# Performance work log

Measured on AMD Instinct MI355X. Metric: run time of the kernel, lower is better.

The kernel has to match this reference:

```python
import jax, jax.numpy as jnp
import numpy as np

IN_FEATURES = 896
OUT_FEATURES = 151936  # Qwen2.5 vocab
BATCH, SEQ = 2, 1024


def setup_inputs() -> dict:
    key = jax.random.key(0)
    k1, k2, k3 = jax.random.split(key, 3)
    x = jax.random.normal(k1, (BATCH, SEQ, IN_FEATURES), dtype=jnp.float32)
    # int8-range quantized weights stored as int32 (values in [-127, 127])
    quant_weight = jax.random.randint(k2, (OUT_FEATURES, IN_FEATURES), -127, 128, dtype=jnp.int32)
    # per-output-row scales (positive, small)
    scales = jax.random.uniform(k3, (OUT_FEATURES,), dtype=jnp.float32, minval=0.001, maxval=0.02)
    return {"x": x, "quant_weight": quant_weight, "scales": scales}


def reference(x, quant_weight, scales):
    # dequantize: W = int8_weight * per_row_scale  -> [out, in]
    w = quant_weight.astype(x.dtype) * scales.astype(x.dtype)[:, None]
    # F.linear(x, W, None) == x @ W.T : [b, s, in] x [out, in] -> [b, s, out]
    return jnp.einsum('bsi,oi->bso', x, w)
```

## Files before the change

kernel.cpp:

```cpp
#include <hip/hip_runtime.h>
#include <hip/hip_bf16.h>


#define M_DIM 2048
#define N_DIM 151936
#define K_DIM 896

#define BM 128
#define BN 128
#define BK 64
#define NKT (K_DIM / BK)
#define MB_CNT (M_DIM / BM)
#define NB_CNT (N_DIM / BN)
#define NWG (MB_CNT * NB_CNT)

typedef __attribute__((ext_vector_type(8))) short bf16x8;
typedef __attribute__((ext_vector_type(4))) float f32x4;
typedef __attribute__((ext_vector_type(4))) int   i32x4;
typedef __attribute__((ext_vector_type(4))) unsigned int u32x4;
typedef __attribute__((ext_vector_type(2))) unsigned int u32x2;

static __device__ __forceinline__ unsigned short f2bf(float f) {
    unsigned int u = __builtin_bit_cast(unsigned int, f);
    u += 0x7FFFu + ((u >> 16) & 1u);
    return (unsigned short)(u >> 16);
}
static __device__ __forceinline__ unsigned int pack2(float lo, float hi) {
    return (unsigned int)f2bf(lo) | ((unsigned int)f2bf(hi) << 16);
}
static __device__ __forceinline__ void gload_lds16(const void* g, void* l) {
    __builtin_amdgcn_global_load_lds(
        (const __attribute__((address_space(1))) unsigned int*)g,
        (__attribute__((address_space(3))) unsigned int*)l, 16, 0, 0);
}


__global__ void quant_x_kernel(const float* __restrict__ X,
                               signed char* __restrict__ Xq,
                               float* __restrict__ Sx) {
    const int row  = blockIdx.x * 4 + (threadIdx.x >> 6);
    const int lane = threadIdx.x & 63;
    const float* xr = X + (size_t)row * K_DIM;
    float v[14];
    float am = 0.f;
    #pragma unroll
    for (int i = 0; i < 14; ++i) {
        v[i] = xr[lane + i * 64];
        am = fmaxf(am, fabsf(v[i]));
    }
    #pragma unroll
    for (int off = 32; off > 0; off >>= 1)
        am = fmaxf(am, __shfl_xor(am, off));
    am = fmaxf(am, 1e-20f);
    const float inv = 127.f / am;
    if (lane == 0) Sx[row] = am / 127.f;
    signed char* qr = Xq + (size_t)row * K_DIM;
    #pragma unroll
    for (int i = 0; i < 14; ++i)
        qr[lane + i * 64] = (signed char)(int)rintf(v[i] * inv);
}

__global__ void cvt_w8_kernel(const int* __restrict__ Wq,
                              signed char* __restrict__ W8) {
    const long n8 = (long)N_DIM * K_DIM / 8;
    for (long i = (long)blockIdx.x * blockDim.x + threadIdx.x; i < n8;
         i += (long)gridDim.x * blockDim.x) {
        i32x4 a = ((const i32x4*)Wq)[2 * i];
        i32x4 b = ((const i32x4*)Wq)[2 * i + 1];
        unsigned int lo = (unsigned int)(a[0] & 0xff) |
                          ((unsigned int)(a[1] & 0xff) << 8) |
                          ((unsigned int)(a[2] & 0xff) << 16) |
                          ((unsigned int)(a[3] & 0xff) << 24);
        unsigned int hi = (unsigned int)(b[0] & 0xff) |
                          ((unsigned int)(b[1] & 0xff) << 8) |
                          ((unsigned int)(b[2] & 0xff) << 16) |
                          ((unsigned int)(b[3] & 0xff) << 24);
        u32x2 o; o[0] = lo; o[1] = hi;
        ((u32x2*)W8)[i] = o;
    }
}


#define SCHED0 __builtin_amdgcn_sched_barrier(0)
#define VMCNT(N) asm volatile("s_waitcnt vmcnt(" #N ")" ::: "memory")
#define LGKM0    asm volatile("s_waitcnt lgkmcnt(0)" ::: "memory")

__global__ __launch_bounds__(256, 3)
void lmhead_gemm_i8(const signed char* __restrict__ Xq,
                    const signed char* __restrict__ W8,
                    const float* __restrict__ Sw,
                    const float* __restrict__ Sx,
                    float* __restrict__ O)
{
    __shared__ signed char lds[3][2][BM][BK];

    const int tid  = threadIdx.x;
    const int lane = tid & 63;
    const int wave = tid >> 6;
    const int wr   = wave >> 1;
    const int wc   = wave & 1;

    const int bid = blockIdx.x;
    const int wg  = (bid & 7) * (NWG / 8) + (bid >> 3);
    const int mb  = wg % MB_CNT;
    const int nb  = wg / MB_CNT;

    const int lslot = (lane & 3) ^ ((lane >> 3) & 3);
    const signed char* srcA0 =
        Xq + (size_t)(mb * BM + wave * 16 + (lane >> 2)) * K_DIM + lslot * 16;
    const signed char* srcA1 = srcA0 + (size_t)64 * K_DIM;
    const signed char* srcB0 =
        W8 + (size_t)(nb * BN + wave * 16 + (lane >> 2)) * K_DIM + lslot * 16;
    const signed char* srcB1 = srcB0 + (size_t)64 * K_DIM;

    auto stage = [&](int b3, int k0) {
        gload_lds16(srcA0 + k0, &lds[b3][0][wave * 16][0]);
        gload_lds16(srcA1 + k0, &lds[b3][0][64 + wave * 16][0]);
        gload_lds16(srcB0 + k0, &lds[b3][1][wave * 16][0]);
        gload_lds16(srcB1 + k0, &lds[b3][1][64 + wave * 16][0]);
    };

    const int physoff   = ((lane >> 4) ^ ((lane >> 1) & 3)) * 16;
    const int arow_base = wr * 64 + (lane & 15);
    const int brow_base = wc * 64 + (lane & 15);

    i32x4 acc[4][4];
    #pragma unroll
    for (int i = 0; i < 4; ++i)
        #pragma unroll
        for (int j = 0; j < 4; ++j)
            acc[i][j] = i32x4{0, 0, 0, 0};

    stage(0, 0);
    stage(1, BK);
    SCHED0;
    VMCNT(0);
    SCHED0;
    __builtin_amdgcn_s_barrier();
    SCHED0;

    i32x4 af[2], bfr[4];

#define READ_A(B3, Q) do { \
    _Pragma("unroll") \
    for (int mf = 0; mf < 2; ++mf) \
        af[mf] = *(const i32x4*)&lds[B3][0][arow_base + (Q)*32 + mf*16][physoff]; \
} while (0)
#define READ_B(B3) do { \
    _Pragma("unroll") \
    for (int nf = 0; nf < 4; ++nf) \
        bfr[nf] = *(const i32x4*)&lds[B3][1][brow_base + nf*16][physoff]; \
} while (0)
#define MFMA_Q(Q) do { \
    __builtin_amdgcn_s_setprio(1); \
    _Pragma("unroll") \
    for (int mf = 0; mf < 2; ++mf) { \
        _Pragma("unroll") \
        for (int nf = 0; nf < 4; ++nf) \
            acc[(Q)*2 + mf][nf] = __builtin_amdgcn_mfma_i32_16x16x64_i8( \
                af[mf], bfr[nf], acc[(Q)*2 + mf][nf], 0, 0, 0); \
    } \
    __builtin_amdgcn_s_setprio(0); \
} while (0)
#define BAR_A() do { SCHED0; __builtin_amdgcn_s_barrier(); SCHED0; } while (0)
#define BAR_B() do { SCHED0; LGKM0; SCHED0; __builtin_amdgcn_s_barrier(); SCHED0; } while (0)

    for (int t = 0; t < NKT - 2; ++t) {
        const int cur = t % 3;
        READ_A(cur, 0); READ_B(cur);
        stage((t + 2) % 3, (t + 2) * BK);
        BAR_A();
        MFMA_Q(0);
        BAR_B();
        READ_A(cur, 1);
        SCHED0;
        VMCNT(4);
        BAR_A();
        MFMA_Q(1);
        BAR_B();
    }

    {
        const int cur = (NKT - 2) % 3;
        READ_A(cur, 0); READ_B(cur);
        BAR_A();
        MFMA_Q(0);
        BAR_B();
        READ_A(cur, 1);
        SCHED0;
        VMCNT(0);
        BAR_A();
        MFMA_Q(1);
        BAR_B();
    }
    {
        const int cur = (NKT - 1) % 3;
        READ_A(cur, 0); READ_B(cur);
        BAR_A();
        MFMA_Q(0);
        BAR_B();
        READ_A(cur, 1);
        BAR_A();
        MFMA_Q(1);
    }

#undef READ_A
#undef READ_B
#undef MFMA_Q
#undef BAR_A
#undef BAR_B

    __syncthreads();

    float* lf = (float*)&lds[0][0][0][0];
    const int qw = lane >> 4;
    const int li = lane & 15;

    float scn[4];
    #pragma unroll
    for (int nf = 0; nf < 4; ++nf)
        scn[nf] = Sw[nb * BN + wc * 64 + nf * 16 + li];

    #pragma unroll
    for (int p = 0; p < 2; ++p) {
        if (p) __syncthreads();
        if (wr == p) {
            #pragma unroll
            for (int a = 0; a < 4; ++a) {
                #pragma unroll
                for (int nf = 0; nf < 4; ++nf) {
                    #pragma unroll
                    for (int r = 0; r < 4; ++r) {
                        const int lr   = a * 16 + qw * 4 + r;
                        const int col  = wc * 64 + nf * 16 + li;
                        const int pcol = col ^ (qw << 4);
                        lf[lr * 128 + pcol] = (float)acc[a][nf][r] * scn[nf];
                    }
                }
            }
        }
        __syncthreads();
        #pragma unroll
        for (int i = 0; i < 8; ++i) {
            const int row = wave * 16 + i * 2 + (lane >> 5);
            const int q   = (row >> 2) & 3;
            const int pch = (lane & 31) ^ (q << 2);
            f32x4 v = *(const f32x4*)&lf[row * 128 + pch * 4];
            const size_t grow = (size_t)(mb * BM + p * 64 + row);
            const float sxr = Sx[grow];
            v *= sxr;
            const size_t gcol = (size_t)(nb * BN + (lane & 31) * 4);
            *(f32x4*)&O[grow * N_DIM + gcol] = v;
        }
    }
}


#define FBM 128
#define FBN 128
#define FBK 32
#define FNSTEPS (K_DIM / FBK)
#define FMB (M_DIM / FBM)
#define FNB (N_DIM / FBN)
#define FNWG (FMB * FNB)

__global__ __launch_bounds__(256, 2)
void lmhead_gemm_conv(const float* __restrict__ X,
                      const int* __restrict__ Wq,
                      const float* __restrict__ S,
                      float* __restrict__ O)
{
    __shared__ unsigned short Alds[2][FBM][FBK];
    __shared__ unsigned short Blds2[2][FBN][FBK];

    const int tid  = threadIdx.x;
    const int lane = tid & 63;
    const int wave = tid >> 6;
    const int wr   = wave >> 1;
    const int wc   = wave & 1;

    const int bid = blockIdx.x;
    const int wg  = (bid & 7) * (FNWG / 8) + (bid >> 3);
    const int mb  = wg % FMB;
    const int nb  = wg / FMB;

    const int srow = tid >> 1;
    const int skh  = (tid & 1) * 16;

    const float* aptr = X  + (size_t)(mb * FBM + srow) * K_DIM + skh;
    const int*   wptr = Wq + (size_t)(nb * FBN + srow) * K_DIM + skh;

    f32x4 av[4];
    i32x4 wv[4];

    auto load_tiles = [&](int k0) {
        const f32x4* ap = (const f32x4*)(aptr + k0);
        const i32x4* wp = (const i32x4*)(wptr + k0);
        av[0] = ap[0]; av[1] = ap[1]; av[2] = ap[2]; av[3] = ap[3];
        wv[0] = wp[0]; wv[1] = wp[1]; wv[2] = wp[2]; wv[3] = wp[3];
    };

    auto stage = [&](int buf) {
        unsigned int apk[8], wpk[8];
        #pragma unroll
        for (int i = 0; i < 8; ++i) {
            apk[i] = pack2(av[(2*i) >> 2][(2*i) & 3], av[(2*i+1) >> 2][(2*i+1) & 3]);
            wpk[i] = pack2((float)wv[(2*i) >> 2][(2*i) & 3], (float)wv[(2*i+1) >> 2][(2*i+1) & 3]);
        }
        *(u32x4*)&Alds[buf][srow][skh]      = u32x4{apk[0], apk[1], apk[2], apk[3]};
        *(u32x4*)&Alds[buf][srow][skh + 8]  = u32x4{apk[4], apk[5], apk[6], apk[7]};
        *(u32x4*)&Blds2[buf][srow][skh]     = u32x4{wpk[0], wpk[1], wpk[2], wpk[3]};
        *(u32x4*)&Blds2[buf][srow][skh + 8] = u32x4{wpk[4], wpk[5], wpk[6], wpk[7]};
    };

    f32x4 acc[4][4];
    #pragma unroll
    for (int i = 0; i < 4; ++i)
        #pragma unroll
        for (int j = 0; j < 4; ++j)
            acc[i][j] = f32x4{0.f, 0.f, 0.f, 0.f};

    load_tiles(0);
    stage(0);
    __syncthreads();

    int cur = 0;
    for (int s = 0; s < FNSTEPS; ++s) {
        if (s + 1 < FNSTEPS) load_tiles((s + 1) * FBK);

        bf16x8 af[4], bfr[4];
        const int arow = wr * 64 + (lane & 15);
        const int brow = wc * 64 + (lane & 15);
        const int kb   = (lane >> 4) * 8;
        #pragma unroll
        for (int mf = 0; mf < 4; ++mf)
            af[mf] = *(const bf16x8*)&Alds[cur][arow + mf * 16][kb];
        #pragma unroll
        for (int nf = 0; nf < 4; ++nf)
            bfr[nf] = *(const bf16x8*)&Blds2[cur][brow + nf * 16][kb];

        #pragma unroll
        for (int mf = 0; mf < 4; ++mf)
            #pragma unroll
            for (int nf = 0; nf < 4; ++nf)
                acc[mf][nf] = __builtin_amdgcn_mfma_f32_16x16x32_bf16(
                    af[mf], bfr[nf], acc[mf][nf], 0, 0, 0);

        if (s + 1 < FNSTEPS) stage(cur ^ 1);
        __syncthreads();
        cur ^= 1;
    }

    #pragma unroll
    for (int nf = 0; nf < 4; ++nf) {
        const int n = nb * FBN + wc * 64 + nf * 16 + (lane & 15);
        const float sc = S[n];
        #pragma unroll
        for (int mf = 0; mf < 4; ++mf) {
            const int m0 = mb * FBM + wr * 64 + mf * 16 + ((lane >> 4) << 2);
            #pragma unroll
            for (int r = 0; r < 4; ++r)
                O[(size_t)(m0 + r) * N_DIM + n] = acc[mf][nf][r] * sc;
        }
    }
}


extern "C" void kernel_launch(void* const* d_in, const int* in_sizes, int n_in,
                              void* d_out, int out_size, void* d_ws, size_t ws_size,
                              hipStream_t stream) {
    const float* X  = (const float*)d_in[0];
    const int*   Wq = (const int*)d_in[1];
    const float* S  = (const float*)d_in[2];
    float*       O  = (float*)d_out;

    const size_t XQ_BYTES = (size_t)M_DIM * K_DIM;
    const size_t SX_BYTES = (size_t)M_DIM * sizeof(float);
    const size_t W8_BYTES = (size_t)N_DIM * K_DIM;

    if (ws_size >= XQ_BYTES + SX_BYTES + W8_BYTES) {
        signed char* xq = (signed char*)d_ws;
        float*       sx = (float*)((char*)d_ws + XQ_BYTES);
        signed char* w8 = (signed char*)((char*)d_ws + XQ_BYTES + SX_BYTES);
        quant_x_kernel<<<M_DIM / 4, 256, 0, stream>>>(X, xq, sx);
        cvt_w8_kernel<<<2048, 256, 0, stream>>>(Wq, w8);
        lmhead_gemm_i8<<<NWG, 256, 0, stream>>>(xq, w8, S, sx, O);
    } else {
        lmhead_gemm_conv<<<FNWG, 256, 0, stream>>>(X, Wq, S, O);
    }
}
```

Before: 707.8 us.

## Collapse ping-pong half-steps into one barrier per K-tile with full fragment loads

Replaces the two-phase per-K-tile schedule, with its four barriers interleaving A-fragment reads and 8-MFMA halves, by a single phase. Each K-tile now loads all 4 A and 4 B fragments, waits on LDS and global counters, passes one barrier and issues 16 MFMAs. The prologue wait is relaxed from vmcnt(0) to vmcnt(4) so the second staged tile can still be in flight. This cuts barrier count and synchronisation stalls. In exchange it holds more fragment registers and loses the interleaving of MFMA work with LDS reads across waves, which could hurt latency hiding.

New measurement: 701.2 us. Within noise of the previous version (-0.9%).

```diff
diff --git a/kernel.cpp b/kernel.cpp
--- a/kernel.cpp
+++ b/kernel.cpp
@@ -134,81 +134,66 @@
     stage(0, 0);
     stage(1, BK);
     SCHED0;
-    VMCNT(0);
+    VMCNT(4);
     SCHED0;
     __builtin_amdgcn_s_barrier();
     SCHED0;
 
-    i32x4 af[2], bfr[4];
-
-#define READ_A(B3, Q) do { \
+    i32x4 af[4], bfr[4];
+
+#define READ_AB(B3) do { \
     _Pragma("unroll") \
-    for (int mf = 0; mf < 2; ++mf) \
-        af[mf] = *(const i32x4*)&lds[B3][0][arow_base + (Q)*32 + mf*16][physoff]; \
-} while (0)
-#define READ_B(B3) do { \
+    for (int mf = 0; mf < 4; ++mf) \
+        af[mf] = *(const i32x4*)&lds[B3][0][arow_base + mf * 16][physoff]; \
     _Pragma("unroll") \
     for (int nf = 0; nf < 4; ++nf) \
-        bfr[nf] = *(const i32x4*)&lds[B3][1][brow_base + nf*16][physoff]; \
+        bfr[nf] = *(const i32x4*)&lds[B3][1][brow_base + nf * 16][physoff]; \
 } while (0)
-#define MFMA_Q(Q) do { \
+#define MFMA16() do { \
     __builtin_amdgcn_s_setprio(1); \
     _Pragma("unroll") \
-    for (int mf = 0; mf < 2; ++mf) { \
+    for (int mf = 0; mf < 4; ++mf) { \
         _Pragma("unroll") \
         for (int nf = 0; nf < 4; ++nf) \
-            acc[(Q)*2 + mf][nf] = __builtin_amdgcn_mfma_i32_16x16x64_i8( \
-                af[mf], bfr[nf], acc[(Q)*2 + mf][nf], 0, 0, 0); \
+            acc[mf][nf] = __builtin_amdgcn_mfma_i32_16x16x64_i8( \
+                af[mf], bfr[nf], acc[mf][nf], 0, 0, 0); \
     } \
     __builtin_amdgcn_s_setprio(0); \
 } while (0)
-#define BAR_A() do { SCHED0; __builtin_amdgcn_s_barrier(); SCHED0; } while (0)
-#define BAR_B() do { SCHED0; LGKM0; SCHED0; __builtin_amdgcn_s_barrier(); SCHED0; } while (0)
 
     for (int t = 0; t < NKT - 2; ++t) {
         const int cur = t % 3;
-        READ_A(cur, 0); READ_B(cur);
+        READ_AB(cur);
         stage((t + 2) % 3, (t + 2) * BK);
-        BAR_A();
-        MFMA_Q(0);
-        BAR_B();
-        READ_A(cur, 1);
         SCHED0;
         VMCNT(4);
-        BAR_A();
-        MFMA_Q(1);
-        BAR_B();
+        LGKM0;
+        SCHED0;
+        __builtin_amdgcn_s_barrier();
+        SCHED0;
+        MFMA16();
     }
 
     {
-        const int cur = (NKT - 2) % 3;
-        READ_A(cur, 0); READ_B(cur);
-        BAR_A();
-        MFMA_Q(0);
-        BAR_B();
-        READ_A(cur, 1);
+        READ_AB((NKT - 2) % 3);
         SCHED0;
         VMCNT(0);
-        BAR_A();
-        MFMA_Q(1);
-        BAR_B();
+        LGKM0;
+        SCHED0;
+        __builtin_amdgcn_s_barrier();
+        SCHED0;
+        MFMA16();
     }
     {
-        const int cur = (NKT - 1) % 3;
-        READ_A(cur, 0); READ_B(cur);
-        BAR_A();
-        MFMA_Q(0);
-        BAR_B();
-        READ_A(cur, 1);
-        BAR_A();
-        MFMA_Q(1);
-    }
-
-#undef READ_A
-#undef READ_B
-#undef MFMA_Q
-#undef BAR_A
-#undef BAR_B
+        READ_AB((NKT - 1) % 3);
+        SCHED0;
+        LGKM0;
+        SCHED0;
+        MFMA16();
+    }
+
+#undef READ_AB
+#undef MFMA16
 
     __syncthreads();
 
```
